# Kernel tuning notes

Hardware: AMD Instinct MI355X
Metric: run time of the kernel (lower is better)

Reference implementation:

```python
import jax, jax.numpy as jnp
import numpy as np

N = 100000
E = 1600000
D_IN, D_HID, D_OUT = 128, 128, 64
SLOPE = 0.01


def setup_inputs() -> dict:
    key = jax.random.key(0)
    k1, k2, k3, k4 = jax.random.split(key, 4)
    x = jax.random.normal(k1, (N, D_IN), dtype=jnp.float32)
    edge_index = jax.random.randint(k2, (2, E), 0, N, dtype=jnp.int64)
    W1 = jax.random.normal(k3, (D_HID, D_IN), dtype=jnp.float32) * 0.05
    b1 = jnp.zeros((D_HID,), dtype=jnp.float32)
    W2 = jax.random.normal(k4, (D_OUT, D_HID), dtype=jnp.float32) * 0.05
    b2 = jnp.zeros((D_OUT,), dtype=jnp.float32)
    return {"x": x, "edge_index": edge_index, "W1": W1, "b1": b1, "W2": W2, "b2": b2}


def _gcn_norm(edge_index, num_nodes):
    # PyG GCNConv: add self loops, symmetric normalization deg^{-1/2} A_hat deg^{-1/2}
    loops = jnp.arange(num_nodes, dtype=edge_index.dtype)
    src = jnp.concatenate([edge_index[0], loops])
    dst = jnp.concatenate([edge_index[1], loops])
    deg = jax.ops.segment_sum(jnp.ones_like(dst, dtype=jnp.float32), dst, num_segments=num_nodes)
    dinv = jnp.where(deg > 0, jax.lax.rsqrt(deg), 0.0)
    norm = dinv[src] * dinv[dst]  # [E+N]
    return src, dst, norm


def _gcn_conv(x, src, dst, norm, W, b):
    h = x @ W.T                              # [N, out]
    msg = h[src] * norm[:, None]             # gather + edge scale: [E+N, out]
    agg = jax.ops.segment_sum(msg, dst, num_segments=x.shape[0])  # scatter-add
    return agg + b


def reference(x, edge_index, W1, b1, W2, b2):
    src, dst, norm = _gcn_norm(edge_index, x.shape[0])
    h1 = jax.nn.leaky_relu(_gcn_conv(x, src, dst, norm, W1, b1), negative_slope=SLOPE)
    h2 = _gcn_conv(h1, src, dst, norm, W2, b2)  # logits, no activation on last layer
    return (h1, h2)
```

## Files before the change

### kernel.cpp

```cpp
#include <hip/hip_runtime.h>


#define THREADS 256

typedef __attribute__((ext_vector_type(8))) short bf16x8;
typedef __attribute__((ext_vector_type(4))) float f32x4;

__device__ __forceinline__ short f2bf_rne(float f) {
    unsigned u = __builtin_bit_cast(unsigned, f);
    u = u + 0x7fffu + ((u >> 16) & 1u);
    return (short)(u >> 16);
}
__device__ __forceinline__ float bf2f(short h) {
    unsigned u = ((unsigned)(unsigned short)h) << 16;
    return __builtin_bit_cast(float, u);
}

__global__ __launch_bounds__(THREADS)
void count_kernel(const int* __restrict__ dst, int* __restrict__ counts, int E) {
    int e = blockIdx.x * THREADS + threadIdx.x;
    if (e < E) atomicAdd(&counts[dst[e]], 1);
}

__global__ __launch_bounds__(THREADS)
void scanA(const int* __restrict__ counts, int* __restrict__ rowptr,
           int* __restrict__ bsum, int n) {
    __shared__ int s[THREADS];
    int i = blockIdx.x * THREADS + threadIdx.x;
    int v = (i < n) ? counts[i] : 0;
    s[threadIdx.x] = v;
    __syncthreads();
    for (int off = 1; off < THREADS; off <<= 1) {
        int a = (threadIdx.x >= off) ? s[threadIdx.x - off] : 0;
        __syncthreads();
        s[threadIdx.x] += a;
        __syncthreads();
    }
    if (i < n) rowptr[i] = s[threadIdx.x] - v;
    if (threadIdx.x == THREADS - 1) bsum[blockIdx.x] = s[threadIdx.x];
}

__global__ __launch_bounds__(512)
void scanB(const int* __restrict__ bsum, int* __restrict__ boff, int nb) {
    __shared__ int s[512];
    int t = threadIdx.x;
    int v = (t < nb) ? bsum[t] : 0;
    s[t] = v;
    __syncthreads();
    for (int off = 1; off < 512; off <<= 1) {
        int a = (t >= off) ? s[t - off] : 0;
        __syncthreads();
        s[t] += a;
        __syncthreads();
    }
    if (t < nb) boff[t] = s[t] - v;
}

__global__ __launch_bounds__(THREADS)
void scanC(int* __restrict__ rowptr, int* __restrict__ cursor, float* __restrict__ dinv,
           const int* __restrict__ counts, const int* __restrict__ boff, int n) {
    int i = blockIdx.x * THREADS + threadIdx.x;
    if (i >= n) return;
    int r = rowptr[i] + boff[blockIdx.x];
    rowptr[i] = r;
    cursor[i] = r;
    dinv[i] = rsqrtf((float)counts[i] + 1.0f);
}

__global__ __launch_bounds__(THREADS)
void fill_kernel(const int* __restrict__ src, const int* __restrict__ dst,
                 int* __restrict__ cursor, int* __restrict__ csr, int E) {
    int e = blockIdx.x * THREADS + threadIdx.x;
    if (e < E) {
        int pos = atomicAdd(&cursor[dst[e]], 1);
        csr[pos] = src[e];
    }
}

template <int DO>
__global__ __launch_bounds__(THREADS)
void gemm_mfma(const float* __restrict__ X, const float* __restrict__ W,
               const float* __restrict__ dinv, float* __restrict__ G, int nrows) {
    constexpr int WCT = DO / 64;
    const int wid = threadIdx.x >> 6;
    const int lane = threadIdx.x & 63;
    const int l15 = lane & 15;
    const int lhi = lane >> 4;

    bf16x8 wh[WCT][4], wl[WCT][4];
#pragma unroll
    for (int ct = 0; ct < WCT; ct++) {
        const int j = (wid * WCT + ct) * 16 + l15;
#pragma unroll
        for (int kc = 0; kc < 4; kc++) {
            const float* wp = W + (size_t)j * 128 + kc * 32 + lhi * 8;
            float4 w0 = *(const float4*)wp;
            float4 w1 = *(const float4*)(wp + 4);
            float wv[8] = {w0.x, w0.y, w0.z, w0.w, w1.x, w1.y, w1.z, w1.w};
#pragma unroll
            for (int t = 0; t < 8; t++) {
                short h = f2bf_rne(wv[t]);
                wh[ct][kc][t] = h;
                wl[ct][kc][t] = f2bf_rne(wv[t] - bf2f(h));
            }
        }
    }

    for (int base = blockIdx.x * 16; base < nrows; base += gridDim.x * 16) {
        const int arow = base + l15;
        const bool av = arow < nrows;
        const float* xp = X + (size_t)arow * 128;
        bf16x8 ah[4], al[4];
#pragma unroll
        for (int kc = 0; kc < 4; kc++) {
            float4 a0 = make_float4(0.f, 0.f, 0.f, 0.f), a1 = a0;
            if (av) {
                a0 = *(const float4*)(xp + kc * 32 + lhi * 8);
                a1 = *(const float4*)(xp + kc * 32 + lhi * 8 + 4);
            }
            float xv[8] = {a0.x, a0.y, a0.z, a0.w, a1.x, a1.y, a1.z, a1.w};
#pragma unroll
            for (int t = 0; t < 8; t++) {
                short h = f2bf_rne(xv[t]);
                ah[kc][t] = h;
                al[kc][t] = f2bf_rne(xv[t] - bf2f(h));
            }
        }

        f32x4 acc[WCT];
#pragma unroll
        for (int ct = 0; ct < WCT; ct++) acc[ct] = (f32x4){0.f, 0.f, 0.f, 0.f};
#pragma unroll
        for (int kc = 0; kc < 4; kc++) {
#pragma unroll
            for (int ct = 0; ct < WCT; ct++) {
                acc[ct] = __builtin_amdgcn_mfma_f32_16x16x32_bf16(ah[kc], wh[ct][kc], acc[ct], 0, 0, 0);
                acc[ct] = __builtin_amdgcn_mfma_f32_16x16x32_bf16(ah[kc], wl[ct][kc], acc[ct], 0, 0, 0);
                acc[ct] = __builtin_amdgcn_mfma_f32_16x16x32_bf16(al[kc], wh[ct][kc], acc[ct], 0, 0, 0);
            }
        }

        float dv[4];
#pragma unroll
        for (int r = 0; r < 4; r++) {
            int row = base + lhi * 4 + r;
            dv[r] = (row < nrows) ? dinv[row] : 0.f;
        }
#pragma unroll
        for (int ct = 0; ct < WCT; ct++) {
            const int j = (wid * WCT + ct) * 16 + l15;
#pragma unroll
            for (int r = 0; r < 4; r++) {
                int row = base + lhi * 4 + r;
                if (row < nrows) G[(size_t)row * DO + j] = dv[r] * acc[ct][r];
            }
        }
    }
}

template <int DO, bool LEAKY>
__global__ __launch_bounds__(THREADS)
void aggregate(const int* __restrict__ rowptr, const int* __restrict__ counts,
               const int* __restrict__ csr, const float* __restrict__ g,
               const float* __restrict__ dinv, const float* __restrict__ bias,
               float* __restrict__ out, int n) {
    int lane = threadIdx.x & 63;
    int node = blockIdx.x * (THREADS / 64) + (threadIdx.x >> 6);
    if (node >= n) return;
    int beg = rowptr[node], cnt = counts[node];

    if (DO == 128) {
        float ax = 0.f, ay = 0.f;
        for (int base = 0; base < cnt; base += 64) {
            int m = cnt - base; if (m > 64) m = 64;
            int sv = (base + lane < cnt) ? csr[beg + base + lane] : 0;
            for (int i = 0; i < m; i++) {
                int s = __shfl(sv, i);
                float2 v = *(const float2*)(g + (size_t)s * 128 + lane * 2);
                ax += v.x; ay += v.y;
            }
        }
        float2 self = *(const float2*)(g + (size_t)node * 128 + lane * 2);
        float2 bv = *(const float2*)(bias + lane * 2);
        float di = dinv[node];
        float rx = di * (ax + self.x) + bv.x;
        float ry = di * (ay + self.y) + bv.y;
        if (LEAKY) {
            rx = rx > 0.f ? rx : 0.01f * rx;
            ry = ry > 0.f ? ry : 0.01f * ry;
        }
        *(float2*)(out + (size_t)node * 128 + lane * 2) = make_float2(rx, ry);
    } else {
        float ax = 0.f;
        for (int base = 0; base < cnt; base += 64) {
            int m = cnt - base; if (m > 64) m = 64;
            int sv = (base + lane < cnt) ? csr[beg + base + lane] : 0;
            for (int i = 0; i < m; i++) {
                int s = __shfl(sv, i);
                ax += g[(size_t)s * 64 + lane];
            }
        }
        float r = dinv[node] * (ax + g[(size_t)node * 64 + lane]) + bias[lane];
        if (LEAKY) r = r > 0.f ? r : 0.01f * r;
        out[(size_t)node * 64 + lane] = r;
    }
}

extern "C" void kernel_launch(void* const* d_in, const int* in_sizes, int n_in,
                              void* d_out, int out_size, void* d_ws, size_t ws_size,
                              hipStream_t stream) {
    const float* x  = (const float*)d_in[0];
    const int*   ei = (const int*)d_in[1];
    const float* W1 = (const float*)d_in[2];
    const float* b1 = (const float*)d_in[3];
    const float* W2 = (const float*)d_in[4];
    const float* b2 = (const float*)d_in[5];

    const int N = in_sizes[0] / 128;
    const int E = in_sizes[1] / 2;
    const int* src = ei;
    const int* dst = ei + E;

    const int NB = (N + THREADS - 1) / THREADS;

    char* ws = (char*)d_ws;
    size_t off = 0;
    auto alloc = [&](size_t bytes) { char* p = ws + off; off = (off + bytes + 511) & ~(size_t)511; return p; };
    int*   counts = (int*)alloc((size_t)N * 4);
    int*   rowptr = (int*)alloc((size_t)N * 4);
    int*   cursor = (int*)alloc((size_t)N * 4);
    int*   bsum   = (int*)alloc((size_t)NB * 4);
    int*   boff   = (int*)alloc((size_t)NB * 4);
    float* dinv   = (float*)alloc((size_t)N * 4);
    int*   csr    = (int*)alloc((size_t)E * 4);
    float* g1     = (float*)alloc((size_t)N * 128 * 4);
    float* g2     = g1;

    float* h1 = (float*)d_out;
    float* h2 = h1 + (size_t)N * 128;

    hipMemsetAsync(counts, 0, (size_t)N * 4, stream);

    const int EB = (E + THREADS - 1) / THREADS;
    count_kernel<<<EB, THREADS, 0, stream>>>(dst, counts, E);
    scanA<<<NB, THREADS, 0, stream>>>(counts, rowptr, bsum, N);
    scanB<<<1, 512, 0, stream>>>(bsum, boff, NB);
    scanC<<<NB, THREADS, 0, stream>>>(rowptr, cursor, dinv, counts, boff, N);
    fill_kernel<<<EB, THREADS, 0, stream>>>(src, dst, cursor, csr, E);

    const int AGB = (N + (THREADS / 64) - 1) / (THREADS / 64);

    gemm_mfma<128><<<2048, THREADS, 0, stream>>>(x, W1, dinv, g1, N);
    aggregate<128, true><<<AGB, THREADS, 0, stream>>>(rowptr, counts, csr, g1, dinv, b1, h1, N);

    gemm_mfma<64><<<2048, THREADS, 0, stream>>>(h1, W2, dinv, g2, N);
    aggregate<64, false><<<AGB, THREADS, 0, stream>>>(rowptr, counts, csr, g2, dinv, b2, h2, N);
}
```

Baseline: 629.4 us.

## Vectorize aggregation with multi-edge float4 gathers and batch graph-build atomics

The aggregation kernels now have each wavefront split into sub-groups that fetch several neighbour rows at once with float4 loads, using four independent accumulators. The partial sums are then reduced across sub-groups with cross-lane shuffles. The aim is more memory-level parallelism and wider loads for the latency-bound gather. The count and fill kernels now process four edges per thread so several loads and atomics are in flight per thread, at the cost of more registers and an extra cross-lane reduction. The first three edge accesses per thread are unguarded, which assumes E is at least three times the thread count.

```diff
diff --git a/kernel.cpp b/kernel.cpp
--- a/kernel.cpp
+++ b/kernel.cpp
@@ -17,9 +17,16 @@
 }
 
 __global__ __launch_bounds__(THREADS)
-void count_kernel(const int* __restrict__ dst, int* __restrict__ counts, int E) {
-    int e = blockIdx.x * THREADS + threadIdx.x;
-    if (e < E) atomicAdd(&counts[dst[e]], 1);
+void count_kernel(const int* __restrict__ dst, int* __restrict__ counts, int E, int T) {
+    int t = blockIdx.x * THREADS + threadIdx.x;
+    int e0 = t, e1 = t + T, e2 = t + 2 * T, e3 = t + 3 * T;
+    int d0 = dst[e0], d1 = dst[e1], d2 = dst[e2];
+    bool v3 = e3 < E;
+    int d3 = v3 ? dst[e3] : 0;
+    atomicAdd(&counts[d0], 1);
+    atomicAdd(&counts[d1], 1);
+    atomicAdd(&counts[d2], 1);
+    if (v3) atomicAdd(&counts[d3], 1);
 }
 
 __global__ __launch_bounds__(THREADS)
@@ -69,12 +76,22 @@
 
 __global__ __launch_bounds__(THREADS)
 void fill_kernel(const int* __restrict__ src, const int* __restrict__ dst,
-                 int* __restrict__ cursor, int* __restrict__ csr, int E) {
-    int e = blockIdx.x * THREADS + threadIdx.x;
-    if (e < E) {
-        int pos = atomicAdd(&cursor[dst[e]], 1);
-        csr[pos] = src[e];
-    }
+                 int* __restrict__ cursor, int* __restrict__ csr, int E, int T) {
+    int t = blockIdx.x * THREADS + threadIdx.x;
+    int e0 = t, e1 = t + T, e2 = t + 2 * T, e3 = t + 3 * T;
+    int d0 = dst[e0], d1 = dst[e1], d2 = dst[e2];
+    int s0 = src[e0], s1 = src[e1], s2 = src[e2];
+    bool v3 = e3 < E;
+    int d3 = v3 ? dst[e3] : 0;
+    int s3 = v3 ? src[e3] : 0;
+    int p0 = atomicAdd(&cursor[d0], 1);
+    int p1 = atomicAdd(&cursor[d1], 1);
+    int p2 = atomicAdd(&cursor[d2], 1);
+    int p3 = v3 ? atomicAdd(&cursor[d3], 1) : 0;
+    csr[p0] = s0;
+    csr[p1] = s1;
+    csr[p2] = s2;
+    if (v3) csr[p3] = s3;
 }
 
 template <int DO>
@@ -164,45 +181,125 @@
                const int* __restrict__ csr, const float* __restrict__ g,
                const float* __restrict__ dinv, const float* __restrict__ bias,
                float* __restrict__ out, int n) {
-    int lane = threadIdx.x & 63;
-    int node = blockIdx.x * (THREADS / 64) + (threadIdx.x >> 6);
+    const int lane = threadIdx.x & 63;
+    const int node = blockIdx.x * (THREADS / 64) + (threadIdx.x >> 6);
     if (node >= n) return;
-    int beg = rowptr[node], cnt = counts[node];
+    const int beg = rowptr[node], cnt = counts[node];
 
     if (DO == 128) {
-        float ax = 0.f, ay = 0.f;
+        const int half = lane >> 5;
+        const int hl = lane & 31;
+        float4 a0 = make_float4(0.f, 0.f, 0.f, 0.f);
+        float4 a1 = a0, a2 = a0, a3 = a0;
         for (int base = 0; base < cnt; base += 64) {
             int m = cnt - base; if (m > 64) m = 64;
             int sv = (base + lane < cnt) ? csr[beg + base + lane] : 0;
-            for (int i = 0; i < m; i++) {
-                int s = __shfl(sv, i);
-                float2 v = *(const float2*)(g + (size_t)s * 128 + lane * 2);
-                ax += v.x; ay += v.y;
-            }
-        }
-        float2 self = *(const float2*)(g + (size_t)node * 128 + lane * 2);
-        float2 bv = *(const float2*)(bias + lane * 2);
-        float di = dinv[node];
-        float rx = di * (ax + self.x) + bv.x;
-        float ry = di * (ay + self.y) + bv.y;
-        if (LEAKY) {
-            rx = rx > 0.f ? rx : 0.01f * rx;
-            ry = ry > 0.f ? ry : 0.01f * ry;
-        }
-        *(float2*)(out + (size_t)node * 128 + lane * 2) = make_float2(rx, ry);
+            int i = 0;
+            for (; i + 8 <= m; i += 8) {
+                int s0 = __shfl(sv, i + half);
+                int s1 = __shfl(sv, i + 2 + half);
+                int s2 = __shfl(sv, i + 4 + half);
+                int s3 = __shfl(sv, i + 6 + half);
+                float4 v0 = *(const float4*)(g + (size_t)s0 * 128 + hl * 4);
+                float4 v1 = *(const float4*)(g + (size_t)s1 * 128 + hl * 4);
+                float4 v2 = *(const float4*)(g + (size_t)s2 * 128 + hl * 4);
+                float4 v3 = *(const float4*)(g + (size_t)s3 * 128 + hl * 4);
+                a0.x += v0.x; a0.y += v0.y; a0.z += v0.z; a0.w += v0.w;
+                a1.x += v1.x; a1.y += v1.y; a1.z += v1.z; a1.w += v1.w;
+                a2.x += v2.x; a2.y += v2.y; a2.z += v2.z; a2.w += v2.w;
+                a3.x += v3.x; a3.y += v3.y; a3.z += v3.z; a3.w += v3.w;
+            }
+            for (; i < m; i += 2) {
+                int idx = i + half;
+                int s = __shfl(sv, idx < m ? idx : 0);
+                if (idx < m) {
+                    float4 v = *(const float4*)(g + (size_t)s * 128 + hl * 4);
+                    a0.x += v.x; a0.y += v.y; a0.z += v.z; a0.w += v.w;
+                }
+            }
+        }
+        a0.x += a1.x + a2.x + a3.x;
+        a0.y += a1.y + a2.y + a3.y;
+        a0.z += a1.z + a2.z + a3.z;
+        a0.w += a1.w + a2.w + a3.w;
+        a0.x += __shfl_xor(a0.x, 32);
+        a0.y += __shfl_xor(a0.y, 32);
+        a0.z += __shfl_xor(a0.z, 32);
+        a0.w += __shfl_xor(a0.w, 32);
+        if (half == 0) {
+            float4 self = *(const float4*)(g + (size_t)node * 128 + hl * 4);
+            float4 bv = ((const float4*)bias)[hl];
+            float di = dinv[node];
+            float4 r;
+            r.x = di * (a0.x + self.x) + bv.x;
+            r.y = di * (a0.y + self.y) + bv.y;
+            r.z = di * (a0.z + self.z) + bv.z;
+            r.w = di * (a0.w + self.w) + bv.w;
+            if (LEAKY) {
+                r.x = r.x > 0.f ? r.x : 0.01f * r.x;
+                r.y = r.y > 0.f ? r.y : 0.01f * r.y;
+                r.z = r.z > 0.f ? r.z : 0.01f * r.z;
+                r.w = r.w > 0.f ? r.w : 0.01f * r.w;
+            }
+            *(float4*)(out + (size_t)node * 128 + hl * 4) = r;
+        }
     } else {
-        float ax = 0.f;
+        const int q = lane >> 4;
+        const int ql = lane & 15;
+        float4 a0 = make_float4(0.f, 0.f, 0.f, 0.f);
+        float4 a1 = a0, a2 = a0, a3 = a0;
         for (int base = 0; base < cnt; base += 64) {
             int m = cnt - base; if (m > 64) m = 64;
             int sv = (base + lane < cnt) ? csr[beg + base + lane] : 0;
-            for (int i = 0; i < m; i++) {
-                int s = __shfl(sv, i);
-                ax += g[(size_t)s * 64 + lane];
-            }
-        }
-        float r = dinv[node] * (ax + g[(size_t)node * 64 + lane]) + bias[lane];
-        if (LEAKY) r = r > 0.f ? r : 0.01f * r;
-        out[(size_t)node * 64 + lane] = r;
+            int i = 0;
+            for (; i + 16 <= m; i += 16) {
+                int s0 = __shfl(sv, i + q);
+                int s1 = __shfl(sv, i + 4 + q);
+                int s2 = __shfl(sv, i + 8 + q);
+                int s3 = __shfl(sv, i + 12 + q);
+                float4 v0 = *(const float4*)(g + (size_t)s0 * 64 + ql * 4);
+                float4 v1 = *(const float4*)(g + (size_t)s1 * 64 + ql * 4);
+                float4 v2 = *(const float4*)(g + (size_t)s2 * 64 + ql * 4);
+                float4 v3 = *(const float4*)(g + (size_t)s3 * 64 + ql * 4);
+                a0.x += v0.x; a0.y += v0.y; a0.z += v0.z; a0.w += v0.w;
+                a1.x += v1.x; a1.y += v1.y; a1.z += v1.z; a1.w += v1.w;
+                a2.x += v2.x; a2.y += v2.y; a2.z += v2.z; a2.w += v2.w;
+                a3.x += v3.x; a3.y += v3.y; a3.z += v3.z; a3.w += v3.w;
+            }
+            for (; i < m; i += 4) {
+                int idx = i + q;
+                int s = __shfl(sv, idx < m ? idx : 0);
+                if (idx < m) {
+                    float4 v = *(const float4*)(g + (size_t)s * 64 + ql * 4);
+                    a0.x += v.x; a0.y += v.y; a0.z += v.z; a0.w += v.w;
+                }
+            }
+        }
+        a0.x += a1.x + a2.x + a3.x;
+        a0.y += a1.y + a2.y + a3.y;
+        a0.z += a1.z + a2.z + a3.z;
+        a0.w += a1.w + a2.w + a3.w;
+        a0.x += __shfl_xor(a0.x, 16); a0.x += __shfl_xor(a0.x, 32);
+        a0.y += __shfl_xor(a0.y, 16); a0.y += __shfl_xor(a0.y, 32);
+        a0.z += __shfl_xor(a0.z, 16); a0.z += __shfl_xor(a0.z, 32);
+        a0.w += __shfl_xor(a0.w, 16); a0.w += __shfl_xor(a0.w, 32);
+        if (q == 0) {
+            float4 self = *(const float4*)(g + (size_t)node * 64 + ql * 4);
+            float4 bv = ((const float4*)bias)[ql];
+            float di = dinv[node];
+            float4 r;
+            r.x = di * (a0.x + self.x) + bv.x;
+            r.y = di * (a0.y + self.y) + bv.y;
+            r.z = di * (a0.z + self.z) + bv.z;
+            r.w = di * (a0.w + self.w) + bv.w;
+            if (LEAKY) {
+                r.x = r.x > 0.f ? r.x : 0.01f * r.x;
+                r.y = r.y > 0.f ? r.y : 0.01f * r.y;
+                r.z = r.z > 0.f ? r.z : 0.01f * r.z;
+                r.w = r.w > 0.f ? r.w : 0.01f * r.w;
+            }
+            *(float4*)(out + (size_t)node * 64 + ql * 4) = r;
+        }
     }
 }
 
@@ -241,12 +338,13 @@
 
     hipMemsetAsync(counts, 0, (size_t)N * 4, stream);
 
-    const int EB = (E + THREADS - 1) / THREADS;
-    count_kernel<<<EB, THREADS, 0, stream>>>(dst, counts, E);
+    const int G4 = (E + 4 * THREADS - 1) / (4 * THREADS);
+    const int T = G4 * THREADS;
+    count_kernel<<<G4, THREADS, 0, stream>>>(dst, counts, E, T);
     scanA<<<NB, THREADS, 0, stream>>>(counts, rowptr, bsum, N);
     scanB<<<1, 512, 0, stream>>>(bsum, boff, NB);
     scanC<<<NB, THREADS, 0, stream>>>(rowptr, cursor, dinv, counts, boff, N);
-    fill_kernel<<<EB, THREADS, 0, stream>>>(src, dst, cursor, csr, E);
+    fill_kernel<<<G4, THREADS, 0, stream>>>(src, dst, cursor, csr, E, T);
 
     const int AGB = (N + (THREADS / 64) - 1) / (THREADS / 64);
 
```

Result: faster. 596.0 us (-5.3%).
